# Performance work log

Measured on AMD Instinct MI355X. Metric: run time of the kernel, lower is better.

The kernel has to match this reference:

```python
import jax, jax.numpy as jnp
import numpy as np

D_MODEL = 1024
D_STATE = 64
D_CONV = 4
EXPAND = 2
INNER = EXPAND * D_STATE          # 128
PROJ = D_STATE + 2 * INNER        # 320
B, L = 8, 4096
EPS = 1e-4


def setup_inputs() -> dict:
    key = jax.random.key(0)
    ks = jax.random.split(key, 6)
    x = jax.random.normal(ks[0], (B, L, D_MODEL), dtype=jnp.float32)
    # depthwise conv weight, torch layout (out=D, in/group=1, K)
    conv_w = jax.random.normal(ks[1], (D_MODEL, 1, D_CONV), dtype=jnp.float32) / np.sqrt(D_CONV)
    conv_b = jnp.zeros((D_MODEL,), dtype=jnp.float32)
    in_proj_w = jax.random.normal(ks[2], (PROJ, D_MODEL), dtype=jnp.float32) / np.sqrt(D_MODEL)
    in_proj_b = jnp.zeros((PROJ,), dtype=jnp.float32)
    A_log = jax.random.normal(ks[3], (D_STATE,), dtype=jnp.float32) * 0.1
    out_proj_w = jax.random.normal(ks[4], (D_MODEL, D_STATE), dtype=jnp.float32) / np.sqrt(D_STATE)
    out_proj_b = jnp.zeros((D_MODEL,), dtype=jnp.float32)
    return {"x": x, "conv_w": conv_w, "conv_b": conv_b,
            "in_proj_w": in_proj_w, "in_proj_b": in_proj_b,
            "A_log": A_log, "out_proj_w": out_proj_w, "out_proj_b": out_proj_b}


def _ssm_forward(x, conv_w, conv_b, in_proj_w, in_proj_b, A_log, out_proj_w, out_proj_b):
    bsz, L_in, _ = x.shape
    # depthwise conv1d, padding (D_CONV-1)//2 on both sides (torch semantics)
    pad = (D_CONV - 1) // 2
    xc = jnp.transpose(x, (0, 2, 1))  # (B, D, L)
    xc = jax.lax.conv_general_dilated(
        xc, conv_w, window_strides=(1,), padding=[(pad, pad)],
        dimension_numbers=("NCH", "OIH", "NCH"), feature_group_count=D_MODEL)
    xc = xc + conv_b[None, :, None]
    Lc = xc.shape[2]
    if Lc < L_in:  # K even -> conv output is L-1; pad zeros on the right
        xc = jnp.pad(xc, ((0, 0), (0, 0), (0, L_in - Lc)))
    elif Lc > L_in:
        xc = xc[:, :, :L_in]
    xc = jnp.transpose(xc, (0, 2, 1))  # (B, L, D)

    proj = xc @ in_proj_w.T + in_proj_b  # (B, L, PROJ)
    delta = proj[..., :D_STATE]                                  # (B, L, N)
    B_in = proj[..., D_STATE:D_STATE + INNER]
    C = proj[..., D_STATE + INNER:]
    n_groups = INNER // D_STATE
    B_in = B_in.reshape(bsz, L_in, D_STATE, n_groups).mean(axis=-1)  # (B, L, N)
    C = C.reshape(bsz, L_in, D_STATE, n_groups).mean(axis=-1)        # (B, L, N)

    # ZOH discretization
    A = -jnp.exp(A_log)[None, None, :]          # (1, 1, N)
    delta = jax.nn.softplus(delta)
    dA = delta * A
    A_bar = jnp.exp(dA)                         # (B, L, N)
    A_safe = jnp.where(jnp.abs(A) < EPS, EPS * jnp.sign(A) + EPS, A)
    scale = (A_bar - 1.0) / A_safe
    taylor = 1.0 + dA / 2.0 + dA * dA / 6.0
    scale = jnp.where(jnp.abs(A) < EPS, taylor, scale)
    B_bar = scale * B_in                        # (B, L, N)

    # linear recurrence h_t = A_bar_t * h_{t-1} + B_bar_t via associative scan
    def comb(e1, e2):
        a1, b1 = e1
        a2, b2 = e2
        return a1 * a2, a2 * b1 + b2
    _, h = jax.lax.associative_scan(comb, (A_bar, B_bar), axis=1)  # (B, L, N)

    y_state = C * h
    return y_state @ out_proj_w.T + out_proj_b  # (B, L, D)


def reference(x, conv_w, conv_b, in_proj_w, in_proj_b, A_log, out_proj_w, out_proj_b):
    return _ssm_forward(x, conv_w, conv_b, in_proj_w, in_proj_b, A_log, out_proj_w, out_proj_b)
```

## Files before the change

### kernel.cpp

```cpp
#include <hip/hip_runtime.h>
#include <cstdint>
#include <cstddef>

typedef __bf16 bf16;
typedef __attribute__((ext_vector_type(4))) __bf16 bf16x4;
typedef __attribute__((ext_vector_type(8))) __bf16 bf16x8;
typedef __attribute__((ext_vector_type(4))) float f32x4;

#define EPS_C 1e-4f
#define SWZ(r) (((r) ^ ((r) >> 2)) & 3)

#define BAR_LDS() do { asm volatile("s_waitcnt lgkmcnt(0)" ::: "memory"); \
                       __builtin_amdgcn_s_barrier(); } while (0)

__global__ __launch_bounds__(256) void k0_prep(const float* __restrict__ Wi,
    const float* __restrict__ Wo, bf16* __restrict__ Whg, bf16* __restrict__ Wlg,
    bf16* __restrict__ Wob, float* __restrict__ zpg)
{
    int idx = blockIdx.x * 256 + threadIdx.x;
    if (idx < 196608) {
        int nn = idx >> 10, k = idx & 1023;
        int wn = nn / 48, s = nn - wn * 48;
        if (s < 16) {
            int d = wn * 16 + s;
            float w = Wi[d * 1024 + k];
            bf16 h = (bf16)w;
            Whg[(k >> 5) * 6144 + nn * 32 + (k & 31)] = h;
            Wlg[(k >> 5) * 2048 + d * 32 + (k & 31)] = (bf16)(w - (float)h);
        } else if (s < 32) {
            int i = wn * 16 + (s - 16);
            float w = 0.5f * (Wi[(64 + 2 * i) * 1024 + k] + Wi[(65 + 2 * i) * 1024 + k]);
            Whg[(k >> 5) * 6144 + nn * 32 + (k & 31)] = (bf16)w;
        } else {
            int i = wn * 16 + (s - 32);
            float w = 0.5f * (Wi[(192 + 2 * i) * 1024 + k] + Wi[(193 + 2 * i) * 1024 + k]);
            Whg[(k >> 5) * 6144 + nn * 32 + (k & 31)] = (bf16)w;
        }
    } else if (idx < 262144) {
        int j = idx - 196608;
        Wob[j] = (bf16)Wo[j];
    } else {
        int j = idx - 262144;
        if (j < 1024) zpg[j] = 0.f;
    }
}

__global__ __launch_bounds__(256) void k1_convproj(
    const float* __restrict__ x, const float* __restrict__ conv_w,
    const float* __restrict__ conv_b, const float* __restrict__ in_proj_b,
    const float* __restrict__ A_log,
    const bf16* __restrict__ Whg, const bf16* __restrict__ Wlg,
    const float* __restrict__ zpg,
    float* __restrict__ Yp, float* __restrict__ Zp,
    float* __restrict__ Psum, float* __restrict__ Ssum)
{
    __shared__ char smem[52224];

    const int tid  = threadIdx.x;
    const int lane = tid & 63;
    const int wn   = tid >> 6;
    const int fr   = lane & 15, fs = lane >> 4;
    const int b    = blockIdx.x >> 6;
    const int tc   = blockIdx.x & 63;
    const int t0   = tc * 64;
    const int rot  = (blockIdx.x * 5) & 31;

    const int tp = tid >> 3, cq = tid & 7;
    const int r0 = tp * 2, r1 = r0 + 1;
    const int gt0 = t0 + r0;
    const bool zrow1 = (gt0 + 1 == 4095);
    const int woff0 = r0 * 80 + cq * 8;
    const int woff1 = r1 * 80 + cq * 8;

    int aoff[4];
#pragma unroll
    for (int mi = 0; mi < 4; ++mi) {
        int r = mi * 16 + fr;
        aoff[mi] = r * 80 + fs * 16;
    }

    const float* rp[5];
#pragma unroll
    for (int dt = 0; dt < 5; ++dt) {
        int g = gt0 - 1 + dt;
        rp[dt] = (g >= 0 && g < 4096) ? (x + ((size_t)b * 4096 + g) * 1024 + cq * 4)
                                      : (zpg + cq * 4);
    }

    const size_t wfo  = (size_t)(wn * 48 + fr) * 32 + fs * 8;
    const size_t wfol = (size_t)(wn * 16 + fr) * 32 + fs * 8;

    {
        float* cwT = (float*)(smem + 20480);
        float* cbl = (float*)(smem + 36864);
        for (int p = tid; p < 1024; p += 256) {
            f32x4 w4 = *(const f32x4*)&conv_w[p * 4];
            cwT[p]        = w4.x;
            cwT[1024 + p] = w4.y;
            cwT[2048 + p] = w4.z;
            cwT[3072 + p] = w4.w;
        }
        ((f32x4*)cbl)[tid] = ((const f32x4*)conv_b)[tid];
    }

    f32x4  xr[5];
    bf16x8 wfh[3], wfl;
    f32x4  acc[4][3] = {};

    auto L = [&](int c) { return (c + rot) & 31; };

    auto fetch_x = [&](int lc) {
#pragma unroll
        for (int dt = 0; dt < 5; ++dt)
            xr[dt] = *(const f32x4*)(rp[dt] + lc * 32);
    };
    auto fetch_w = [&](int lc) {
        const bf16* ph = Whg + (size_t)lc * 6144 + wfo;
#pragma unroll
        for (int ni = 0; ni < 3; ++ni)
            wfh[ni] = *(const bf16x8*)(ph + ni * 512);
        wfl = *(const bf16x8*)(Wlg + (size_t)lc * 2048 + wfol);
    };
    auto conv = [&](int lc, int p) {
        char* xh = smem + p * 5120;
        char* xl = smem + 10240 + p * 5120;
        const float* cwT = (const float*)(smem + 20480);
        const float* cbl = (const float*)(smem + 36864);
        const int ch0 = lc * 32 + cq * 4;
        f32x4 w0 = *(const f32x4*)&cwT[ch0];
        f32x4 w1 = *(const f32x4*)&cwT[1024 + ch0];
        f32x4 w2 = *(const f32x4*)&cwT[2048 + ch0];
        f32x4 w3 = *(const f32x4*)&cwT[3072 + ch0];
        f32x4 bb = *(const f32x4*)&cbl[ch0];
        bf16x4 hi0, lo0, hi1, lo1;
#pragma unroll
        for (int j = 0; j < 4; ++j) {
            float v0 = bb[j];
            v0 = fmaf(w0[j], xr[0][j], v0);
            v0 = fmaf(w1[j], xr[1][j], v0);
            v0 = fmaf(w2[j], xr[2][j], v0);
            v0 = fmaf(w3[j], xr[3][j], v0);
            float v1 = bb[j];
            v1 = fmaf(w0[j], xr[1][j], v1);
            v1 = fmaf(w1[j], xr[2][j], v1);
            v1 = fmaf(w2[j], xr[3][j], v1);
            v1 = fmaf(w3[j], xr[4][j], v1);
            v1 = zrow1 ? 0.f : v1;
            bf16 h0 = (bf16)v0, h1 = (bf16)v1;
            hi0[j] = h0; lo0[j] = (bf16)(v0 - (float)h0);
            hi1[j] = h1; lo1[j] = (bf16)(v1 - (float)h1);
        }
        *(bf16x4*)(xh + woff0) = hi0;
        *(bf16x4*)(xh + woff1) = hi1;
        *(bf16x4*)(xl + woff0) = lo0;
        *(bf16x4*)(xl + woff1) = lo1;
    };

    fetch_x(L(0));
    fetch_w(L(0));
    __syncthreads();
    conv(L(0), 0);
    fetch_x(L(1));
    __syncthreads();

    auto body = [&](int c, int par) {
        const char* xh = smem + par * 5120;
        const char* xl = smem + 10240 + par * 5120;
        bf16x8 ah[4], al[4];
#pragma unroll
        for (int mi = 0; mi < 4; ++mi) {
            ah[mi] = *(const bf16x8*)(xh + aoff[mi]);
            al[mi] = *(const bf16x8*)(xl + aoff[mi]);
        }
        __builtin_amdgcn_s_setprio(1);
#pragma unroll
        for (int ni = 0; ni < 3; ++ni) {
            bf16x8 bh = wfh[ni];
#pragma unroll
            for (int mi = 0; mi < 4; ++mi)
                acc[mi][ni] = __builtin_amdgcn_mfma_f32_16x16x32_bf16(ah[mi], bh, acc[mi][ni], 0, 0, 0);
#pragma unroll
            for (int mi = 0; mi < 4; ++mi)
                acc[mi][ni] = __builtin_amdgcn_mfma_f32_16x16x32_bf16(al[mi], bh, acc[mi][ni], 0, 0, 0);
        }
#pragma unroll
        for (int mi = 0; mi < 4; ++mi)
            acc[mi][0] = __builtin_amdgcn_mfma_f32_16x16x32_bf16(ah[mi], wfl, acc[mi][0], 0, 0, 0);
        __builtin_amdgcn_s_setprio(0);
        if (c + 1 < 32) {
            fetch_w(L(c + 1));
            conv(L(c + 1), par ^ 1);
            if (c + 2 < 32) fetch_x(L(c + 2));
        }
        BAR_LDS();
    };

#pragma unroll 1
    for (int cc = 0; cc < 32; cc += 2) {
        body(cc,     0);
        body(cc + 1, 1);
    }

    float* res = (float*)smem;
#pragma unroll
    for (int mi = 0; mi < 4; ++mi)
#pragma unroll
        for (int ni = 0; ni < 3; ++ni) {
            int col = wn * 48 + ni * 16 + fr;
#pragma unroll
            for (int r = 0; r < 4; ++r)
                res[(mi * 16 + fs * 4 + r) * 196 + col] = acc[mi][ni][r];
        }
    __syncthreads();

    float* part = (float*)(smem + 50176);
    const int i  = lane;
    const int tg = tid >> 6;
    const float A  = -expf(A_log[i]);
    const float bd = in_proj_b[i];
    const float bB = 0.5f * (in_proj_b[64 + 2 * i] + in_proj_b[65 + 2 * i]);
    const float bC = 0.5f * (in_proj_b[192 + 2 * i] + in_proj_b[193 + 2 * i]);
    const bool tiny = fabsf(A) < EPS_C;
    const int dcol = (i >> 4) * 48 + (i & 15);
    float av[16], bv[16], cv[16];
#pragma unroll
    for (int r = 0; r < 16; ++r) {
        int t = tg * 16 + r;
        float d  = res[t * 196 + dcol] + bd;
        float Bm = res[t * 196 + dcol + 16] + bB;
        float Cm = res[t * 196 + dcol + 32] + bC;
        float delta = (d > 20.f) ? d : log1pf(expf(d));
        float dA = delta * A;
        float abar = expf(dA);
        float sc = tiny ? (1.f + dA * 0.5f + dA * dA * (1.f / 6.f)) : ((abar - 1.f) / A);
        av[r] = abar; bv[r] = sc * Bm; cv[r] = Cm;
    }
    float P = 1.f, S = 0.f;
#pragma unroll
    for (int r = 0; r < 16; ++r) { S = fmaf(av[r], S, bv[r]); P *= av[r]; }
    part[tg * 64 + i] = P;
    part[256 + tg * 64 + i] = S;
    __syncthreads();
    float h = 0.f, pp = 1.f;
#pragma unroll
    for (int g = 0; g < 3; ++g)
        if (g < tg) {
            float Pg = part[g * 64 + i], Sg = part[256 + g * 64 + i];
            h = fmaf(Pg, h, Sg);
            pp *= Pg;
        }
    size_t ob = ((size_t)b * 4096 + t0 + tg * 16) * 64 + i;
#pragma unroll
    for (int r = 0; r < 16; ++r) {
        h  = fmaf(av[r], h, bv[r]);
        pp *= av[r];
        Yp[ob + (size_t)r * 64] = cv[r] * h;
        Zp[ob + (size_t)r * 64] = cv[r] * pp;
    }
    if (tg == 3) {
        size_t o = ((size_t)b * 64 + tc) * 64 + i;
        Psum[o] = pp;
        Ssum[o] = h;
    }
}

__global__ __launch_bounds__(64) void k2_scan2(const float* __restrict__ Psum,
    const float* __restrict__ Ssum, float* __restrict__ Carry)
{
    int b = blockIdx.x, i = threadIdx.x;
    float Pv[64], Sv[64];
#pragma unroll
    for (int c = 0; c < 64; ++c) {
        size_t o = ((size_t)(b * 64) + c) * 64 + i;
        Pv[c] = Psum[o]; Sv[c] = Ssum[o];
    }
    float h = 0.f;
#pragma unroll
    for (int c = 0; c < 64; ++c) {
        size_t o = ((size_t)(b * 64) + c) * 64 + i;
        Carry[o] = h;
        h = fmaf(Pv[c], h, Sv[c]);
    }
}

__global__ __launch_bounds__(512) void k3_scan_out(
    const float* __restrict__ Yp, const float* __restrict__ Zp,
    const float* __restrict__ Carry, const bf16* __restrict__ Wob,
    const float* __restrict__ bo, float* __restrict__ out)
{
    __shared__ char sm3[8192];

    const int tid  = threadIdx.x;
    const int lane = tid & 63;
    const int wv   = tid >> 6;
    const int b    = blockIdx.x >> 6;
    const int ch   = blockIdx.x & 63;
    const int t0   = ch * 64;

    const int i = lane, tg = wv;
    float cr = Carry[((size_t)(b * 64) + ch) * 64 + i];
    size_t base = ((size_t)(b * 4096) + t0 + tg * 8) * 64 + i;
#pragma unroll
    for (int r = 0; r < 8; ++r) {
        float y = Yp[base + (size_t)r * 64] + Zp[base + (size_t)r * 64] * cr;
        int t = tg * 8 + r;
        int off = t * 128 + ((((i >> 3) ^ (t & 7)) & 7) << 4) + (i & 7) * 2;
        *(bf16*)(sm3 + off) = (bf16)y;
    }
    __syncthreads();

    const int fr = lane & 15, fs = lane >> 4;
    bf16x8 afr[4][2];
#pragma unroll
    for (int mi = 0; mi < 4; ++mi)
#pragma unroll
        for (int ks = 0; ks < 2; ++ks) {
            int row = mi * 16 + fr;
            int slot = ks * 4 + fs;
            int off = row * 128 + (((slot ^ (row & 7)) & 7) << 4);
            afr[mi][ks] = *(const bf16x8*)(sm3 + off);
        }
    const int n0 = wv * 128;
#pragma unroll
    for (int ni = 0; ni < 8; ++ni) {
        int col = n0 + ni * 16 + fr;
        bf16x8 b0 = *(const bf16x8*)(Wob + (size_t)col * 64 + fs * 8);
        bf16x8 b1 = *(const bf16x8*)(Wob + (size_t)col * 64 + 32 + fs * 8);
        float bias = bo[col];
#pragma unroll
        for (int mi = 0; mi < 4; ++mi) {
            f32x4 a = {};
            a = __builtin_amdgcn_mfma_f32_16x16x32_bf16(afr[mi][0], b0, a, 0, 0, 0);
            a = __builtin_amdgcn_mfma_f32_16x16x32_bf16(afr[mi][1], b1, a, 0, 0, 0);
#pragma unroll
            for (int r = 0; r < 4; ++r) {
                int t = mi * 16 + fs * 4 + r;
                out[((size_t)(b * 4096) + t0 + t) * 1024 + col] = a[r] + bias;
            }
        }
    }
}

extern "C" void kernel_launch(void* const* d_in, const int* in_sizes, int n_in,
                              void* d_out, int out_size, void* d_ws, size_t ws_size,
                              hipStream_t stream) {
    const float* x          = (const float*)d_in[0];
    const float* conv_w     = (const float*)d_in[1];
    const float* conv_b     = (const float*)d_in[2];
    const float* in_proj_w  = (const float*)d_in[3];
    const float* in_proj_b  = (const float*)d_in[4];
    const float* A_log      = (const float*)d_in[5];
    const float* out_proj_w = (const float*)d_in[6];
    const float* out_proj_b = (const float*)d_in[7];
    float* out = (float*)d_out;

    char* w = (char*)d_ws;
    bf16*  Whg  = (bf16*)w;
    bf16*  Wlg  = (bf16*)(w + 393216);
    bf16*  Wob  = (bf16*)(w + 524288);
    float* Yp   = (float*)(w + 655360);
    float* Zp   = (float*)(w + 9043968);
    float* Psum = (float*)(w + 17432576);
    float* Ssum = (float*)(w + 17563648);
    float* Carry= (float*)(w + 17694720);
    float* zpg  = (float*)(w + 17825792);

    hipLaunchKernelGGL(k0_prep,     dim3(1032), dim3(256), 0, stream,
                       in_proj_w, out_proj_w, Whg, Wlg, Wob, zpg);
    hipLaunchKernelGGL(k1_convproj, dim3(512),  dim3(256), 0, stream,
                       x, conv_w, conv_b, in_proj_b, A_log, Whg, Wlg, zpg,
                       Yp, Zp, Psum, Ssum);
    hipLaunchKernelGGL(k2_scan2,    dim3(8),    dim3(64),  0, stream, Psum, Ssum, Carry);
    hipLaunchKernelGGL(k3_scan_out, dim3(512),  dim3(512), 0, stream,
                       Yp, Zp, Carry, Wob, out_proj_b, out);
}
```

Before: 95.78 us.

## Double k1 time tile to 128 rows with 8 waves and pack Y/Z intermediates as fp16

k1_convproj now runs 512-thread blocks, each covering 128 timesteps with two wave groups sharing the same weight fragments. This halves weight fetches per row and the number of blocks, and the scan epilogue is done in two 64-row halves through the shared result buffer. The Y and Z intermediates are stored as a packed fp16 pair instead of two fp32 arrays, cutting intermediate traffic between k1 and k3. The trade-offs are lower fp16 precision for the scan outputs (Z is a cumulative product that may underflow), half as many blocks (256) for the GPU's CUs, and more registers per thread.

```diff
diff --git a/kernel.cpp b/kernel.cpp
--- a/kernel.cpp
+++ b/kernel.cpp
@@ -6,6 +6,7 @@
 typedef __attribute__((ext_vector_type(4))) __bf16 bf16x4;
 typedef __attribute__((ext_vector_type(8))) __bf16 bf16x8;
 typedef __attribute__((ext_vector_type(4))) float f32x4;
+typedef __attribute__((ext_vector_type(2))) _Float16 f16x2;
 
 #define EPS_C 1e-4f
 #define SWZ(r) (((r) ^ ((r) >> 2)) & 3)
@@ -45,24 +46,25 @@
     }
 }
 
-__global__ __launch_bounds__(256) void k1_convproj(
+__global__ __launch_bounds__(512) void k1_convproj(
     const float* __restrict__ x, const float* __restrict__ conv_w,
     const float* __restrict__ conv_b, const float* __restrict__ in_proj_b,
     const float* __restrict__ A_log,
     const bf16* __restrict__ Whg, const bf16* __restrict__ Wlg,
     const float* __restrict__ zpg,
-    float* __restrict__ Yp, float* __restrict__ Zp,
+    f16x2* __restrict__ YZp,
     float* __restrict__ Psum, float* __restrict__ Ssum)
 {
-    __shared__ char smem[52224];
+    __shared__ char smem[61440];
 
     const int tid  = threadIdx.x;
     const int lane = tid & 63;
-    const int wn   = tid >> 6;
+    const int wv   = tid >> 6;
+    const int wt   = wv >> 2, wn = wv & 3;
     const int fr   = lane & 15, fs = lane >> 4;
-    const int b    = blockIdx.x >> 6;
-    const int tc   = blockIdx.x & 63;
-    const int t0   = tc * 64;
+    const int b    = blockIdx.x >> 5;
+    const int tc   = blockIdx.x & 31;
+    const int t0   = tc * 128;
     const int rot  = (blockIdx.x * 5) & 31;
 
     const int tp = tid >> 3, cq = tid & 7;
@@ -75,7 +77,7 @@
     int aoff[4];
 #pragma unroll
     for (int mi = 0; mi < 4; ++mi) {
-        int r = mi * 16 + fr;
+        int r = wt * 64 + mi * 16 + fr;
         aoff[mi] = r * 80 + fs * 16;
     }
 
@@ -91,16 +93,16 @@
     const size_t wfol = (size_t)(wn * 16 + fr) * 32 + fs * 8;
 
     {
-        float* cwT = (float*)(smem + 20480);
-        float* cbl = (float*)(smem + 36864);
-        for (int p = tid; p < 1024; p += 256) {
+        float* cwT = (float*)(smem + 40960);
+        float* cbl = (float*)(smem + 57344);
+        for (int p = tid; p < 1024; p += 512) {
             f32x4 w4 = *(const f32x4*)&conv_w[p * 4];
             cwT[p]        = w4.x;
             cwT[1024 + p] = w4.y;
             cwT[2048 + p] = w4.z;
             cwT[3072 + p] = w4.w;
         }
-        ((f32x4*)cbl)[tid] = ((const f32x4*)conv_b)[tid];
+        if (tid < 256) ((f32x4*)cbl)[tid] = ((const f32x4*)conv_b)[tid];
     }
 
     f32x4  xr[5];
@@ -122,10 +124,10 @@
         wfl = *(const bf16x8*)(Wlg + (size_t)lc * 2048 + wfol);
     };
     auto conv = [&](int lc, int p) {
-        char* xh = smem + p * 5120;
-        char* xl = smem + 10240 + p * 5120;
-        const float* cwT = (const float*)(smem + 20480);
-        const float* cbl = (const float*)(smem + 36864);
+        char* xh = smem + p * 10240;
+        char* xl = smem + 20480 + p * 10240;
+        const float* cwT = (const float*)(smem + 40960);
+        const float* cbl = (const float*)(smem + 57344);
         const int ch0 = lc * 32 + cq * 4;
         f32x4 w0 = *(const f32x4*)&cwT[ch0];
         f32x4 w1 = *(const f32x4*)&cwT[1024 + ch0];
@@ -164,8 +166,8 @@
     __syncthreads();
 
     auto body = [&](int c, int par) {
-        const char* xh = smem + par * 5120;
-        const char* xl = smem + 10240 + par * 5120;
+        const char* xh = smem + par * 10240;
+        const char* xl = smem + 20480 + par * 10240;
         bf16x8 ah[4], al[4];
 #pragma unroll
         for (int mi = 0; mi < 4; ++mi) {
@@ -201,18 +203,7 @@
         body(cc + 1, 1);
     }
 
-    float* res = (float*)smem;
-#pragma unroll
-    for (int mi = 0; mi < 4; ++mi)
-#pragma unroll
-        for (int ni = 0; ni < 3; ++ni) {
-            int col = wn * 48 + ni * 16 + fr;
-#pragma unroll
-            for (int r = 0; r < 4; ++r)
-                res[(mi * 16 + fs * 4 + r) * 196 + col] = acc[mi][ni][r];
-        }
-    __syncthreads();
-
+    float* res  = (float*)smem;
     float* part = (float*)(smem + 50176);
     const int i  = lane;
     const int tg = tid >> 6;
@@ -222,45 +213,64 @@
     const float bC = 0.5f * (in_proj_b[192 + 2 * i] + in_proj_b[193 + 2 * i]);
     const bool tiny = fabsf(A) < EPS_C;
     const int dcol = (i >> 4) * 48 + (i & 15);
-    float av[16], bv[16], cv[16];
-#pragma unroll
-    for (int r = 0; r < 16; ++r) {
-        int t = tg * 16 + r;
-        float d  = res[t * 196 + dcol] + bd;
-        float Bm = res[t * 196 + dcol + 16] + bB;
-        float Cm = res[t * 196 + dcol + 32] + bC;
-        float delta = (d > 20.f) ? d : log1pf(expf(d));
-        float dA = delta * A;
-        float abar = expf(dA);
-        float sc = tiny ? (1.f + dA * 0.5f + dA * dA * (1.f / 6.f)) : ((abar - 1.f) / A);
-        av[r] = abar; bv[r] = sc * Bm; cv[r] = Cm;
-    }
-    float P = 1.f, S = 0.f;
-#pragma unroll
-    for (int r = 0; r < 16; ++r) { S = fmaf(av[r], S, bv[r]); P *= av[r]; }
-    part[tg * 64 + i] = P;
-    part[256 + tg * 64 + i] = S;
-    __syncthreads();
-    float h = 0.f, pp = 1.f;
-#pragma unroll
-    for (int g = 0; g < 3; ++g)
-        if (g < tg) {
-            float Pg = part[g * 64 + i], Sg = part[256 + g * 64 + i];
-            h = fmaf(Pg, h, Sg);
-            pp *= Pg;
-        }
-    size_t ob = ((size_t)b * 4096 + t0 + tg * 16) * 64 + i;
-#pragma unroll
-    for (int r = 0; r < 16; ++r) {
-        h  = fmaf(av[r], h, bv[r]);
-        pp *= av[r];
-        Yp[ob + (size_t)r * 64] = cv[r] * h;
-        Zp[ob + (size_t)r * 64] = cv[r] * pp;
-    }
-    if (tg == 3) {
-        size_t o = ((size_t)b * 64 + tc) * 64 + i;
-        Psum[o] = pp;
-        Ssum[o] = h;
+
+#pragma unroll 1
+    for (int hh = 0; hh < 2; ++hh) {
+        __syncthreads();
+        if (wt == hh) {
+#pragma unroll
+            for (int mi = 0; mi < 4; ++mi)
+#pragma unroll
+                for (int ni = 0; ni < 3; ++ni) {
+                    int col = wn * 48 + ni * 16 + fr;
+#pragma unroll
+                    for (int r = 0; r < 4; ++r)
+                        res[(mi * 16 + fs * 4 + r) * 196 + col] = acc[mi][ni][r];
+                }
+        }
+        __syncthreads();
+        float av[8], bv[8], cv[8];
+#pragma unroll
+        for (int r = 0; r < 8; ++r) {
+            int t = tg * 8 + r;
+            float d  = res[t * 196 + dcol] + bd;
+            float Bm = res[t * 196 + dcol + 16] + bB;
+            float Cm = res[t * 196 + dcol + 32] + bC;
+            float delta = (d > 20.f) ? d : log1pf(expf(d));
+            float dA = delta * A;
+            float abar = expf(dA);
+            float sc = tiny ? (1.f + dA * 0.5f + dA * dA * (1.f / 6.f)) : ((abar - 1.f) / A);
+            av[r] = abar; bv[r] = sc * Bm; cv[r] = Cm;
+        }
+        float P = 1.f, S = 0.f;
+#pragma unroll
+        for (int r = 0; r < 8; ++r) { S = fmaf(av[r], S, bv[r]); P *= av[r]; }
+        part[tg * 64 + i] = P;
+        part[512 + tg * 64 + i] = S;
+        __syncthreads();
+        float h = 0.f, pp = 1.f;
+#pragma unroll
+        for (int g = 0; g < 7; ++g)
+            if (g < tg) {
+                float Pg = part[g * 64 + i], Sg = part[512 + g * 64 + i];
+                h = fmaf(Pg, h, Sg);
+                pp *= Pg;
+            }
+        size_t ob = ((size_t)b * 4096 + t0 + hh * 64 + tg * 8) * 64 + i;
+#pragma unroll
+        for (int r = 0; r < 8; ++r) {
+            h  = fmaf(av[r], h, bv[r]);
+            pp *= av[r];
+            f16x2 yz;
+            yz[0] = (_Float16)(cv[r] * h);
+            yz[1] = (_Float16)(cv[r] * pp);
+            YZp[ob + (size_t)r * 64] = yz;
+        }
+        if (tg == 7) {
+            size_t o = ((size_t)b * 64 + tc * 2 + hh) * 64 + i;
+            Psum[o] = pp;
+            Ssum[o] = h;
+        }
     }
 }
 
@@ -284,9 +294,9 @@
 }
 
 __global__ __launch_bounds__(512) void k3_scan_out(
-    const float* __restrict__ Yp, const float* __restrict__ Zp,
-    const float* __restrict__ Carry, const bf16* __restrict__ Wob,
-    const float* __restrict__ bo, float* __restrict__ out)
+    const f16x2* __restrict__ YZp, const float* __restrict__ Carry,
+    const bf16* __restrict__ Wob, const float* __restrict__ bo,
+    float* __restrict__ out)
 {
     __shared__ char sm3[8192];
 
@@ -302,7 +312,8 @@
     size_t base = ((size_t)(b * 4096) + t0 + tg * 8) * 64 + i;
 #pragma unroll
     for (int r = 0; r < 8; ++r) {
-        float y = Yp[base + (size_t)r * 64] + Zp[base + (size_t)r * 64] * cr;
+        f16x2 yz = YZp[base + (size_t)r * 64];
+        float y = (float)yz[0] + (float)yz[1] * cr;
         int t = tg * 8 + r;
         int off = t * 128 + ((((i >> 3) ^ (t & 7)) & 7) << 4) + (i & 7) * 2;
         *(bf16*)(sm3 + off) = (bf16)y;
@@ -358,19 +369,18 @@
     bf16*  Whg  = (bf16*)w;
     bf16*  Wlg  = (bf16*)(w + 393216);
     bf16*  Wob  = (bf16*)(w + 524288);
-    float* Yp   = (float*)(w + 655360);
-    float* Zp   = (float*)(w + 9043968);
-    float* Psum = (float*)(w + 17432576);
-    float* Ssum = (float*)(w + 17563648);
-    float* Carry= (float*)(w + 17694720);
-    float* zpg  = (float*)(w + 17825792);
+    f16x2* YZp  = (f16x2*)(w + 655360);
+    float* Psum = (float*)(w + 9043968);
+    float* Ssum = (float*)(w + 9175040);
+    float* Carry= (float*)(w + 9306112);
+    float* zpg  = (float*)(w + 9437184);
 
     hipLaunchKernelGGL(k0_prep,     dim3(1032), dim3(256), 0, stream,
                        in_proj_w, out_proj_w, Whg, Wlg, Wob, zpg);
-    hipLaunchKernelGGL(k1_convproj, dim3(512),  dim3(256), 0, stream,
+    hipLaunchKernelGGL(k1_convproj, dim3(256),  dim3(512), 0, stream,
                        x, conv_w, conv_b, in_proj_b, A_log, Whg, Wlg, zpg,
-                       Yp, Zp, Psum, Ssum);
+                       YZp, Psum, Ssum);
     hipLaunchKernelGGL(k2_scan2,    dim3(8),    dim3(64),  0, stream, Psum, Ssum, Carry);
     hipLaunchKernelGGL(k3_scan_out, dim3(512),  dim3(512), 0, stream,
-                       Yp, Zp, Carry, Wob, out_proj_b, out);
-}
+                       YZp, Carry, Wob, out_proj_b, out);
+}
```

Result: faster. 91.16 us (-4.8%).
